# Kernel tuning notes

Measured on AMD Instinct MI355X. Metric: run time of the kernel, lower is better.

The kernel has to match this reference:

```python
import jax, jax.numpy as jnp
import numpy as np

B, N, C = 4, 49152, 256
E = 393216
CMID = C // 4
K = 3
EPS = 1e-5


def _cheb_prop(x, row, col, a_norm):
    # L_hat x with lambda_max=2, sym norm: L_hat = -D^{-1/2} A D^{-1/2} (zero diag)
    # x: [B, N, F]
    msg = a_norm[None, :, None] * x[:, col, :]           # [B, E, F]
    return -jnp.zeros_like(x).at[:, row, :].add(msg)


def _cheb_conv(x, row, col, a_norm, W, b):
    # W: [K, Fin, Fout], b: [Fout]
    out = jnp.einsum('bnf,fg->bng', x, W[0])
    Tx0, Tx1 = x, _cheb_prop(x, row, col, a_norm)
    out = out + jnp.einsum('bnf,fg->bng', Tx1, W[1])
    for k in range(2, W.shape[0]):
        Tx2 = 2.0 * _cheb_prop(Tx1, row, col, a_norm) - Tx0
        out = out + jnp.einsum('bnf,fg->bng', Tx2, W[k])
        Tx0, Tx1 = Tx1, Tx2
    return out + b


def _inst_norm(y):
    # InstanceNorm over the node axis (y viewed as [B, C, N]), affine=False
    mean = jnp.mean(y, axis=1, keepdims=True)
    var = jnp.var(y, axis=1, keepdims=True)
    return (y - mean) * jax.lax.rsqrt(var + EPS)


def setup_inputs() -> dict:
    key = jax.random.key(0)
    ks = jax.random.split(key, 8)
    x = jax.random.normal(ks[0], (B, N, C), dtype=jnp.float32)
    edge_index = jax.random.randint(ks[1], (2, E), 0, N, dtype=jnp.int32)
    edge_weight = jax.random.uniform(ks[2], (E,), dtype=jnp.float32)
    s1 = 1.0 / np.sqrt(C)
    s2 = 1.0 / np.sqrt(CMID)
    W1 = jax.random.normal(ks[3], (K, C, CMID), dtype=jnp.float32) * s1
    W2 = jax.random.normal(ks[4], (K, CMID, CMID), dtype=jnp.float32) * s2
    W3 = jax.random.normal(ks[5], (K, CMID, C), dtype=jnp.float32) * s2
    b1 = jnp.zeros((CMID,), dtype=jnp.float32)
    b2 = jnp.zeros((CMID,), dtype=jnp.float32)
    b3 = jnp.zeros((C,), dtype=jnp.float32)
    return {"x": x, "edge_index": edge_index, "edge_weight": edge_weight,
            "W1": W1, "b1": b1, "W2": W2, "b2": b2, "W3": W3, "b3": b3}


def reference(x, edge_index, edge_weight, W1, b1, W2, b2, W3, b3):
    row, col = edge_index[0], edge_index[1]
    deg = jnp.zeros((N,), dtype=x.dtype).at[row].add(edge_weight)
    dinv = jnp.where(deg > 0, jax.lax.rsqrt(jnp.maximum(deg, EPS)), 0.0)
    a_norm = edge_weight * dinv[row] * dinv[col]

    y = _cheb_conv(x, row, col, a_norm, W1, b1)
    y = jax.nn.relu(_inst_norm(y))
    y = _cheb_conv(y, row, col, a_norm, W2, b2)
    y = jax.nn.relu(_inst_norm(y))
    y = _cheb_conv(y, row, col, a_norm, W3, b3)
    y = jax.nn.relu(_inst_norm(y))
    return y + x
```

## Files before the change

### kernel.cpp

```cpp
#include <hip/hip_runtime.h>

#define NNODES 49152
#define NB 4
#define NE 393216
#define MTOT (NB*NNODES)
#define EPS 1e-5f

typedef __attribute__((ext_vector_type(8))) short s8v;
typedef __attribute__((ext_vector_type(4))) float f32x4;

__device__ inline float b2f(ushort u){ union{uint i; float f;} v; v.i = ((uint)u)<<16; return v.f; }
__device__ inline ushort f2b(float f){ union{float f; uint i;} v; v.f=f; uint r = v.i + 0x7fff + ((v.i>>16)&1); return (ushort)(r>>16); }

__global__ __launch_bounds__(256) void k_deg_cnt(const int* __restrict__ row,
    const float* __restrict__ w, float* __restrict__ deg, int* __restrict__ cnt)
{
    int e = blockIdx.x*256 + threadIdx.x;
    if (e >= NE) return;
    int r = row[e];
    atomicAdd(&deg[r], w[e]);
    atomicAdd(&cnt[r], 1);
}

__global__ __launch_bounds__(256) void k_dinv(const float* __restrict__ deg, float* __restrict__ dinv)
{
    int i = blockIdx.x*256 + threadIdx.x;
    if (i >= NNODES) return;
    float d = deg[i];
    dinv[i] = (d > 0.0f) ? rsqrtf(fmaxf(d, EPS)) : 0.0f;
}

__global__ __launch_bounds__(1024) void k_scan(const int* __restrict__ cnt, int* __restrict__ rowptr)
{
    __shared__ int ssum[1024];
    const int CH = NNODES/1024;
    int t = threadIdx.x;
    int base = t*CH;
    int loc[CH];
    int s = 0;
    #pragma unroll
    for (int i = 0; i < CH; ++i) { loc[i] = s; s += cnt[base+i]; }
    ssum[t] = s;
    __syncthreads();
    for (int off = 1; off < 1024; off <<= 1) {
        int v = ssum[t];
        int add = (t >= off) ? ssum[t-off] : 0;
        __syncthreads();
        ssum[t] = v + add;
        __syncthreads();
    }
    int prefix = (t == 0) ? 0 : ssum[t-1];
    #pragma unroll
    for (int i = 0; i < CH; ++i) rowptr[base+i] = prefix + loc[i];
    if (t == 0) rowptr[NNODES] = ssum[1023];
}

__global__ __launch_bounds__(256) void k_fill(const int* __restrict__ row, const int* __restrict__ col,
    const float* __restrict__ w, const float* __restrict__ dinv,
    const int* __restrict__ rowptr, int* __restrict__ fill,
    int* __restrict__ ecol, float* __restrict__ ea)
{
    int e = blockIdx.x*256 + threadIdx.x;
    if (e >= NE) return;
    int r = row[e], c = col[e];
    int pos = rowptr[r] + atomicAdd(&fill[r], 1);
    ecol[pos] = c;
    ea[pos] = w[e] * dinv[r] * dinv[c];
}

__global__ __launch_bounds__(256) void k_packB(const float* __restrict__ W, int Fin, int NF, int K,
    int mode, ushort* __restrict__ out)
{
    int t = blockIdx.x*256 + threadIdx.x;
    int lane = t & 63;
    int fid = t >> 6;
    if (fid >= (K/32)*NF) return;
    int kb = fid / NF, nb = fid % NF;
    int kbase = kb*32 + ((lane>>4)<<3);
    int n0 = nb*16 + (lane&15);
    #pragma unroll
    for (int j = 0; j < 8; ++j) {
        int kk = kbase + j;
        float v;
        if (mode == 0) {
            if (n0 < 64)       v = W[kk*64 + n0] - W[2*Fin*64 + kk*64 + n0];
            else if (n0 < 128) v = W[Fin*64 + kk*64 + (n0-64)];
            else               v = W[2*Fin*64 + kk*64 + (n0-128)];
        } else {
            v = W[(kk>>6)*64*256 + (kk&63)*256 + n0];
        }
        out[((long)fid*64 + lane)*8 + j] = f2b(v);
    }
}

__global__ __launch_bounds__(256) void k_gemm1(const float* __restrict__ A,
    const ushort* __restrict__ Bp, ushort* __restrict__ C0, ushort* __restrict__ C1, ushort* __restrict__ C2)
{
    int tid = threadIdx.x;
    int w = tid >> 6, l = tid & 63;
    int lr = l & 15, kg = l >> 4;
    int n0 = blockIdx.x * 32;
    f32x4 acc[2][12];
    #pragma unroll
    for (int rf = 0; rf < 2; ++rf)
        #pragma unroll
        for (int nb = 0; nb < 12; ++nb) acc[rf][nb] = (f32x4){0.f,0.f,0.f,0.f};

    for (int kt = 0; kt < 256; kt += 32) {
        s8v afr[2];
        #pragma unroll
        for (int rf = 0; rf < 2; ++rf) {
            long rowg = (long)w*NNODES + n0 + rf*16 + lr;
            const float* af = A + rowg*256 + kt + (kg<<3);
            float4 v0 = *(const float4*)af;
            float4 v1 = *(const float4*)(af + 4);
            s8v fr;
            fr[0]=(short)f2b(v0.x); fr[1]=(short)f2b(v0.y); fr[2]=(short)f2b(v0.z); fr[3]=(short)f2b(v0.w);
            fr[4]=(short)f2b(v1.x); fr[5]=(short)f2b(v1.y); fr[6]=(short)f2b(v1.z); fr[7]=(short)f2b(v1.w);
            afr[rf] = fr;
        }
        const ushort* bb = Bp + ((long)(kt>>5)*12)*512 + l*8;
        #pragma unroll
        for (int nb = 0; nb < 12; ++nb) {
            s8v bfr = *(const s8v*)(bb + nb*512);
            acc[0][nb] = __builtin_amdgcn_mfma_f32_16x16x32_bf16(afr[0], bfr, acc[0][nb], 0, 0, 0);
            acc[1][nb] = __builtin_amdgcn_mfma_f32_16x16x32_bf16(afr[1], bfr, acc[1][nb], 0, 0, 0);
        }
    }
    #pragma unroll
    for (int rf = 0; rf < 2; ++rf) {
        #pragma unroll
        for (int nb = 0; nb < 12; ++nb) {
            ushort* arr = (nb < 4) ? C0 : ((nb < 8) ? C1 : C2);
            #pragma unroll
            for (int i = 0; i < 4; ++i) {
                long crow = ((long)(n0 + rf*16 + kg*4 + i))*4 + w;
                arr[crow*64 + (nb&3)*16 + lr] = f2b(acc[rf][nb][i]);
            }
        }
    }
}

__global__ __launch_bounds__(256) void k_gemm2(const ushort* __restrict__ A,
    const ushort* __restrict__ Bp, ushort* __restrict__ C0, ushort* __restrict__ C1, ushort* __restrict__ C2)
{
    int tid = threadIdx.x;
    int w = tid >> 6, l = tid & 63;
    int lr = l & 15, kg = l >> 4;
    long rb = (long)blockIdx.x * 128;
    f32x4 acc[2][12];
    #pragma unroll
    for (int rf = 0; rf < 2; ++rf)
        #pragma unroll
        for (int nb = 0; nb < 12; ++nb) acc[rf][nb] = (f32x4){0.f,0.f,0.f,0.f};

    #pragma unroll
    for (int kt = 0; kt < 64; kt += 32) {
        s8v afr[2];
        #pragma unroll
        for (int rf = 0; rf < 2; ++rf) {
            long rg = rb + w*32 + rf*16 + lr;
            afr[rf] = *(const s8v*)(A + rg*64 + kt + (kg<<3));
        }
        const ushort* bb = Bp + ((long)(kt>>5)*12)*512 + l*8;
        #pragma unroll
        for (int nb = 0; nb < 12; ++nb) {
            s8v bfr = *(const s8v*)(bb + nb*512);
            acc[0][nb] = __builtin_amdgcn_mfma_f32_16x16x32_bf16(afr[0], bfr, acc[0][nb], 0, 0, 0);
            acc[1][nb] = __builtin_amdgcn_mfma_f32_16x16x32_bf16(afr[1], bfr, acc[1][nb], 0, 0, 0);
        }
    }
    #pragma unroll
    for (int rf = 0; rf < 2; ++rf) {
        #pragma unroll
        for (int nb = 0; nb < 12; ++nb) {
            ushort* arr = (nb < 4) ? C0 : ((nb < 8) ? C1 : C2);
            #pragma unroll
            for (int i = 0; i < 4; ++i) {
                long crow = rb + w*32 + rf*16 + kg*4 + i;
                arr[crow*64 + (nb&3)*16 + lr] = f2b(acc[rf][nb][i]);
            }
        }
    }
}

__global__ __launch_bounds__(256) void k_gemm3(const ushort* __restrict__ A0,
    const ushort* __restrict__ A1, const ushort* __restrict__ A2,
    const ushort* __restrict__ Bp, ushort* __restrict__ C, float* __restrict__ Pst)
{
    int tid = threadIdx.x;
    int w = tid >> 6, l = tid & 63;
    int lr = l & 15, kg = l >> 4;
    long rb = (long)blockIdx.x * 128;
    f32x4 acc[2][16];
    #pragma unroll
    for (int rf = 0; rf < 2; ++rf)
        #pragma unroll
        for (int nb = 0; nb < 16; ++nb) acc[rf][nb] = (f32x4){0.f,0.f,0.f,0.f};

    for (int kt = 0; kt < 192; kt += 32) {
        int part = kt >> 6, kc = kt & 63;
        const ushort* Ap = (part == 0) ? A0 : ((part == 1) ? A1 : A2);
        s8v afr[2];
        #pragma unroll
        for (int rf = 0; rf < 2; ++rf) {
            long rg = rb + w*32 + rf*16 + lr;
            afr[rf] = *(const s8v*)(Ap + rg*64 + kc + (kg<<3));
        }
        const ushort* bb = Bp + ((long)(kt>>5)*16)*512 + l*8;
        #pragma unroll
        for (int nb = 0; nb < 16; ++nb) {
            s8v bfr = *(const s8v*)(bb + nb*512);
            acc[0][nb] = __builtin_amdgcn_mfma_f32_16x16x32_bf16(afr[0], bfr, acc[0][nb], 0, 0, 0);
            acc[1][nb] = __builtin_amdgcn_mfma_f32_16x16x32_bf16(afr[1], bfr, acc[1][nb], 0, 0, 0);
        }
    }
    #pragma unroll
    for (int rf = 0; rf < 2; ++rf) {
        #pragma unroll
        for (int nb = 0; nb < 16; ++nb) {
            #pragma unroll
            for (int i = 0; i < 4; ++i) {
                long crow = rb + w*32 + rf*16 + kg*4 + i;
                C[crow*256 + nb*16 + lr] = f2b(acc[rf][nb][i]);
            }
        }
    }
    __shared__ float Ls[4][4][256];
    __shared__ float Lq[4][4][256];
    #pragma unroll
    for (int nb = 0; nb < 16; ++nb) {
        #pragma unroll
        for (int i = 0; i < 4; ++i) {
            float x0 = acc[0][nb][i], x1 = acc[1][nb][i];
            float s = x0 + x1;
            float q = x0*x0 + x1*x1;
            s += __shfl_xor(s, 16); s += __shfl_xor(s, 32);
            q += __shfl_xor(q, 16); q += __shfl_xor(q, 32);
            if (kg == 0) { Ls[w][i][nb*16 + lr] = s; Lq[w][i][nb*16 + lr] = q; }
        }
    }
    __syncthreads();
    int t = tid;
    #pragma unroll
    for (int b = 0; b < 4; ++b) {
        float S = Ls[0][b][t] + Ls[1][b][t] + Ls[2][b][t] + Ls[3][b][t];
        float Q = Lq[0][b][t] + Lq[1][b][t] + Lq[2][b][t] + Lq[3][b][t];
        Pst[(long)blockIdx.x*2048 + b*256 + t] = S;
        Pst[(long)blockIdx.x*2048 + 1024 + b*256 + t] = Q;
    }
}

__global__ __launch_bounds__(256) void k_prop(
    const int* __restrict__ rowptr, const int* __restrict__ ecol, const float* __restrict__ ea,
    const ushort* __restrict__ src, const ushort* __restrict__ basep, float beta,
    ushort* __restrict__ dst, float alpha, float* __restrict__ Pst)
{
    int g = blockIdx.x*8 + (threadIdx.x >> 5);
    int sub = threadIdx.x & 31;
    int e0 = rowptr[g], e1 = rowptr[g+1];
    float acc[8];
    #pragma unroll
    for (int j = 0; j < 8; ++j) acc[j] = 0.f;
    int e = e0;
    for (; e + 4 <= e1; e += 4) {
        int c0 = ecol[e], c1 = ecol[e+1], c2 = ecol[e+2], c3 = ecol[e+3];
        float a0 = ea[e], a1 = ea[e+1], a2 = ea[e+2], a3 = ea[e+3];
        s8v v0 = *(const s8v*)(src + (long)c0*256 + sub*8);
        s8v v1 = *(const s8v*)(src + (long)c1*256 + sub*8);
        s8v v2 = *(const s8v*)(src + (long)c2*256 + sub*8);
        s8v v3 = *(const s8v*)(src + (long)c3*256 + sub*8);
        #pragma unroll
        for (int j = 0; j < 8; ++j)
            acc[j] += a0*b2f((ushort)v0[j]) + a1*b2f((ushort)v1[j])
                    + a2*b2f((ushort)v2[j]) + a3*b2f((ushort)v3[j]);
    }
    for (; e < e1; ++e) {
        int c = ecol[e]; float a = ea[e];
        s8v v = *(const s8v*)(src + (long)c*256 + sub*8);
        #pragma unroll
        for (int j = 0; j < 8; ++j) acc[j] += a*b2f((ushort)v[j]);
    }
    float o[8];
    if (basep) {
        s8v bv = *(const s8v*)(basep + (long)g*256 + sub*8);
        #pragma unroll
        for (int j = 0; j < 8; ++j) o[j] = alpha*acc[j] + beta*b2f((ushort)bv[j]);
    } else {
        #pragma unroll
        for (int j = 0; j < 8; ++j) o[j] = alpha*acc[j];
    }
    s8v ov;
    #pragma unroll
    for (int j = 0; j < 8; ++j) ov[j] = (short)f2b(o[j]);
    *(s8v*)(dst + (long)g*256 + sub*8) = ov;

    if (Pst) {
        __shared__ float Ls[8][256];
        __shared__ float Lq[8][256];
        int grp = threadIdx.x >> 5;
        #pragma unroll
        for (int j = 0; j < 8; ++j) {
            Ls[grp][sub*8 + j] = o[j];
            Lq[grp][sub*8 + j] = o[j]*o[j];
        }
        __syncthreads();
        int t = threadIdx.x;
        float s = 0.f, q = 0.f;
        #pragma unroll
        for (int k = 0; k < 8; ++k) { s += Ls[k][t]; q += Lq[k][t]; }
        Pst[(long)blockIdx.x*512 + t] = s;
        Pst[(long)blockIdx.x*512 + 256 + t] = q;
    }
}

__global__ __launch_bounds__(256) void k_redgen(const float* __restrict__ in, float* __restrict__ out,
    int S, int nin)
{
    int j = blockIdx.x*256 + threadIdx.x;
    int o = blockIdx.y;
    long base = (long)o*nin*S + j;
    float s = 0.f;
    for (int k = 0; k < nin; ++k) s += in[base + (long)k*S];
    out[(long)o*S + j] = s;
}

__global__ __launch_bounds__(256) void k_redfin(const float* __restrict__ in, int S, int nin, int Cw,
    float* __restrict__ mean, float* __restrict__ rs)
{
    int half = S >> 1;
    int j = blockIdx.x*256 + threadIdx.x;
    if (j >= half) return;
    float s = 0.f, q = 0.f;
    for (int k = 0; k < nin; ++k) {
        s += in[(long)k*S + j];
        q += in[(long)k*S + half + j];
    }
    float m = s / (float)NNODES;
    float v = q / (float)NNODES - m*m;
    int b = j / Cw, c = j - b*Cw;
    mean[b*256 + c] = m;
    rs[b*256 + c] = rsqrtf(v + EPS);
}

__global__ __launch_bounds__(256) void k_normrelu(const ushort* __restrict__ y,
    const float* __restrict__ mean, const float* __restrict__ rs, ushort* __restrict__ X)
{
    int t = threadIdx.x;
    long e = (long)blockIdx.x*2048 + t*8;
    int b = (t>>3)&3, c0 = (t&7)*8;
    s8v v = *(const s8v*)(y + e);
    float4 m0 = *(const float4*)(mean + b*256 + c0);
    float4 m1 = *(const float4*)(mean + b*256 + c0 + 4);
    float4 r0 = *(const float4*)(rs + b*256 + c0);
    float4 r1 = *(const float4*)(rs + b*256 + c0 + 4);
    float mm[8] = {m0.x,m0.y,m0.z,m0.w,m1.x,m1.y,m1.z,m1.w};
    float rr[8] = {r0.x,r0.y,r0.z,r0.w,r1.x,r1.y,r1.z,r1.w};
    s8v o;
    #pragma unroll
    for (int j = 0; j < 8; ++j) o[j] = (short)f2b(fmaxf((b2f((ushort)v[j]) - mm[j])*rr[j], 0.f));
    *(s8v*)(X + e) = o;
}

__global__ __launch_bounds__(256) void k_final(const ushort* __restrict__ Ybf,
    const float* __restrict__ x, const float* __restrict__ mean, const float* __restrict__ rs,
    float* __restrict__ out)
{
    int t = threadIdx.x;
    long orow = (long)blockIdx.x*8 + (t>>5);
    int c0 = (t&31)*8;
    int b = (int)(orow / NNODES);
    int n = (int)(orow - (long)b*NNODES);
    s8v v = *(const s8v*)(Ybf + ((long)n*4 + b)*256 + c0);
    float4 m0 = *(const float4*)(mean + b*256 + c0);
    float4 m1 = *(const float4*)(mean + b*256 + c0 + 4);
    float4 r0 = *(const float4*)(rs + b*256 + c0);
    float4 r1 = *(const float4*)(rs + b*256 + c0 + 4);
    float mm[8] = {m0.x,m0.y,m0.z,m0.w,m1.x,m1.y,m1.z,m1.w};
    float rr[8] = {r0.x,r0.y,r0.z,r0.w,r1.x,r1.y,r1.z,r1.w};
    const float* xp = x + orow*256 + c0;
    float* op = out + orow*256 + c0;
    #pragma unroll
    for (int j = 0; j < 8; ++j)
        op[j] = fmaxf((b2f((ushort)v[j]) - mm[j])*rr[j], 0.f) + xp[j];
}

extern "C" void kernel_launch(void* const* d_in, const int* in_sizes, int n_in,
                              void* d_out, int out_size, void* d_ws, size_t ws_size,
                              hipStream_t stream)
{
    const float* x  = (const float*)d_in[0];
    const int*   ei = (const int*)d_in[1];
    const float* ew = (const float*)d_in[2];
    const float* W1 = (const float*)d_in[3];
    const float* W2 = (const float*)d_in[5];
    const float* W3 = (const float*)d_in[7];
    const int* row = ei;
    const int* col = ei + NE;

    char* p = (char*)d_ws;
    size_t used = 0;
    auto alloc = [&](size_t bytes) -> void* {
        void* r = p + used;
        used += (bytes + 1023) & ~(size_t)1023;
        return r;
    };
    float* deg   = (float*)alloc((size_t)3*NNODES*4);
    int*   cnt   = (int*)(deg + NNODES);
    int*   fillc = (int*)(deg + 2*NNODES);
    float* dinv  = (float*)alloc((size_t)NNODES*4);
    int*   rowptr= (int*)alloc((size_t)(NNODES+1)*4);
    int*   ecol  = (int*)alloc((size_t)NE*4);
    float* ea    = (float*)alloc((size_t)NE*4);
    float* mrs   = (float*)alloc((size_t)3*2*1024*4);
    ushort* Bp1  = (ushort*)alloc((size_t)256*192*2);
    ushort* Bp2  = (ushort*)alloc((size_t)64*192*2);
    ushort* Bp3  = (ushort*)alloc((size_t)192*256*2);
    ushort* Za   = (ushort*)alloc((size_t)MTOT*64*2);
    ushort* Zb   = (ushort*)alloc((size_t)MTOT*64*2);
    ushort* Zc   = (ushort*)alloc((size_t)MTOT*64*2);
    ushort* Zd   = (ushort*)alloc((size_t)MTOT*64*2);
    float* Pbig  = (float*)alloc((size_t)6144*512*4);
    float* PPa   = (float*)alloc((size_t)256*2048*4);
    float* PPb   = (float*)alloc((size_t)16*2048*4);
    ushort* Ybf  = (ushort*)alloc((size_t)MTOT*256*2);
    if (ws_size < used) return;

    float* mean1 = mrs;          float* rs1 = mrs + 1024;
    float* mean2 = mrs + 2048;   float* rs2 = mrs + 3072;
    float* mean3 = mrs + 4096;   float* rs3 = mrs + 5120;

    hipMemsetAsync(deg, 0, (size_t)3*NNODES*4, stream);
    k_deg_cnt<<<NE/256, 256, 0, stream>>>(row, ew, deg, cnt);
    k_dinv<<<NNODES/256, 256, 0, stream>>>(deg, dinv);
    k_scan<<<1, 1024, 0, stream>>>(cnt, rowptr);
    k_fill<<<NE/256, 256, 0, stream>>>(row, col, ew, dinv, rowptr, fillc, ecol, ea);
    k_packB<<<24, 256, 0, stream>>>(W1, 256, 12, 256, 0, Bp1);
    k_packB<<<6, 256, 0, stream>>>(W2, 64, 12, 64, 0, Bp2);
    k_packB<<<24, 256, 0, stream>>>(W3, 64, 16, 192, 1, Bp3);

    k_gemm1<<<NNODES/32, 256, 0, stream>>>(x, Bp1, Za, Zb, Zc);
    k_prop<<<NNODES/8, 256, 0, stream>>>(rowptr, ecol, ea, Zc, Zb, 1.f, Zb, -2.f, nullptr);
    k_prop<<<NNODES/8, 256, 0, stream>>>(rowptr, ecol, ea, Zb, Za, 1.f, Za, -1.f, Pbig);
    k_redgen<<<dim3(2,512), 256, 0, stream>>>(Pbig, PPa, 512, 12);
    k_redgen<<<dim3(2,32), 256, 0, stream>>>(PPa, PPb, 512, 16);
    k_redfin<<<1, 256, 0, stream>>>(PPb, 512, 32, 64, mean1, rs1);
    k_normrelu<<<MTOT*64/2048, 256, 0, stream>>>(Za, mean1, rs1, Zc);

    k_gemm2<<<MTOT/128, 256, 0, stream>>>(Zc, Bp2, Za, Zb, Zd);
    k_prop<<<NNODES/8, 256, 0, stream>>>(rowptr, ecol, ea, Zd, Zb, 1.f, Zb, -2.f, nullptr);
    k_prop<<<NNODES/8, 256, 0, stream>>>(rowptr, ecol, ea, Zb, Za, 1.f, Za, -1.f, Pbig);
    k_redgen<<<dim3(2,512), 256, 0, stream>>>(Pbig, PPa, 512, 12);
    k_redgen<<<dim3(2,32), 256, 0, stream>>>(PPa, PPb, 512, 16);
    k_redfin<<<1, 256, 0, stream>>>(PPb, 512, 32, 64, mean2, rs2);
    k_normrelu<<<MTOT*64/2048, 256, 0, stream>>>(Za, mean2, rs2, Zc);

    k_prop<<<NNODES/8, 256, 0, stream>>>(rowptr, ecol, ea, Zc, (const ushort*)nullptr, 0.f, Za, -1.f, nullptr);
    k_prop<<<NNODES/8, 256, 0, stream>>>(rowptr, ecol, ea, Za, Zc, -1.f, Zb, -2.f, nullptr);
    k_gemm3<<<MTOT/128, 256, 0, stream>>>(Zc, Za, Zb, Bp3, Ybf, Pbig);
    k_redgen<<<dim3(8,256), 256, 0, stream>>>(Pbig, PPa, 2048, 6);
    k_redgen<<<dim3(8,16), 256, 0, stream>>>(PPa, PPb, 2048, 16);
    k_redfin<<<4, 256, 0, stream>>>(PPb, 2048, 16, 256, mean3, rs3);
    k_final<<<MTOT/8, 256, 0, stream>>>(Ybf, x, mean3, rs3, (float*)d_out);
}
```

Before: 717.0 us.

## Stage GEMM weights in double-buffered LDS and halve per-block row tiles

All three GEMM kernels now stage the packed weight matrix in shared memory, double-buffered with register prefetch for gemm1 and gemm3, instead of each wave reading B fragments from global memory. Each block now covers half as many rows (one 16-row fragment per wave), and launch bounds request three blocks per SM. This lowers register pressure, raises occupancy and cuts redundant global B traffic, at the cost of more blocks and more syncs. The gemm3 partial-stat buffer moves into the output buffer, which doubles the partial count fed to the reduction.

```diff
diff --git a/kernel.cpp b/kernel.cpp
--- a/kernel.cpp
+++ b/kernel.cpp
@@ -93,161 +93,185 @@
     }
 }
 
-__global__ __launch_bounds__(256) void k_gemm1(const float* __restrict__ A,
+__global__ __launch_bounds__(256,3) void k_gemm1(const float* __restrict__ A,
     const ushort* __restrict__ Bp, ushort* __restrict__ C0, ushort* __restrict__ C1, ushort* __restrict__ C2)
 {
+    __shared__ ushort Bs[2][6144];
     int tid = threadIdx.x;
     int w = tid >> 6, l = tid & 63;
     int lr = l & 15, kg = l >> 4;
-    int n0 = blockIdx.x * 32;
-    f32x4 acc[2][12];
-    #pragma unroll
-    for (int rf = 0; rf < 2; ++rf)
-        #pragma unroll
-        for (int nb = 0; nb < 12; ++nb) acc[rf][nb] = (f32x4){0.f,0.f,0.f,0.f};
-
-    for (int kt = 0; kt < 256; kt += 32) {
-        s8v afr[2];
-        #pragma unroll
-        for (int rf = 0; rf < 2; ++rf) {
-            long rowg = (long)w*NNODES + n0 + rf*16 + lr;
-            const float* af = A + rowg*256 + kt + (kg<<3);
-            float4 v0 = *(const float4*)af;
-            float4 v1 = *(const float4*)(af + 4);
-            s8v fr;
-            fr[0]=(short)f2b(v0.x); fr[1]=(short)f2b(v0.y); fr[2]=(short)f2b(v0.z); fr[3]=(short)f2b(v0.w);
-            fr[4]=(short)f2b(v1.x); fr[5]=(short)f2b(v1.y); fr[6]=(short)f2b(v1.z); fr[7]=(short)f2b(v1.w);
-            afr[rf] = fr;
-        }
-        const ushort* bb = Bp + ((long)(kt>>5)*12)*512 + l*8;
+    int n0 = blockIdx.x * 16;
+
+    const float* ap = A + ((long)w*NNODES + n0 + lr)*256 + (kg<<3);
+    s8v af[8];
+    #pragma unroll
+    for (int t = 0; t < 8; ++t) {
+        float4 v0 = *(const float4*)(ap + t*32);
+        float4 v1 = *(const float4*)(ap + t*32 + 4);
+        s8v fr;
+        fr[0]=(short)f2b(v0.x); fr[1]=(short)f2b(v0.y); fr[2]=(short)f2b(v0.z); fr[3]=(short)f2b(v0.w);
+        fr[4]=(short)f2b(v1.x); fr[5]=(short)f2b(v1.y); fr[6]=(short)f2b(v1.z); fr[7]=(short)f2b(v1.w);
+        af[t] = fr;
+    }
+    f32x4 acc[12];
+    #pragma unroll
+    for (int nb = 0; nb < 12; ++nb) acc[nb] = (f32x4){0.f,0.f,0.f,0.f};
+
+    #pragma unroll
+    for (int ps = 0; ps < 3; ++ps) {
+        int off = ps*2048 + tid*8;
+        *(s8v*)(&Bs[0][off]) = *(const s8v*)(Bp + off);
+    }
+    #pragma unroll
+    for (int t = 0; t < 8; ++t) {
+        __syncthreads();
+        s8v stg[3];
+        if (t < 7) {
+            #pragma unroll
+            for (int ps = 0; ps < 3; ++ps)
+                stg[ps] = *(const s8v*)(Bp + (long)(t+1)*6144 + ps*2048 + tid*8);
+        }
+        const ushort* bb = &Bs[t&1][l*8];
         #pragma unroll
         for (int nb = 0; nb < 12; ++nb) {
             s8v bfr = *(const s8v*)(bb + nb*512);
-            acc[0][nb] = __builtin_amdgcn_mfma_f32_16x16x32_bf16(afr[0], bfr, acc[0][nb], 0, 0, 0);
-            acc[1][nb] = __builtin_amdgcn_mfma_f32_16x16x32_bf16(afr[1], bfr, acc[1][nb], 0, 0, 0);
-        }
-    }
-    #pragma unroll
-    for (int rf = 0; rf < 2; ++rf) {
-        #pragma unroll
-        for (int nb = 0; nb < 12; ++nb) {
-            ushort* arr = (nb < 4) ? C0 : ((nb < 8) ? C1 : C2);
+            acc[nb] = __builtin_amdgcn_mfma_f32_16x16x32_bf16(af[t], bfr, acc[nb], 0, 0, 0);
+        }
+        if (t < 7) {
             #pragma unroll
-            for (int i = 0; i < 4; ++i) {
-                long crow = ((long)(n0 + rf*16 + kg*4 + i))*4 + w;
-                arr[crow*64 + (nb&3)*16 + lr] = f2b(acc[rf][nb][i]);
-            }
-        }
-    }
-}
-
-__global__ __launch_bounds__(256) void k_gemm2(const ushort* __restrict__ A,
+            for (int ps = 0; ps < 3; ++ps)
+                *(s8v*)(&Bs[(t+1)&1][ps*2048 + tid*8]) = stg[ps];
+        }
+    }
+    #pragma unroll
+    for (int nb = 0; nb < 12; ++nb) {
+        ushort* arr = (nb < 4) ? C0 : ((nb < 8) ? C1 : C2);
+        int cc = (nb&3)*16 + lr;
+        #pragma unroll
+        for (int i = 0; i < 4; ++i) {
+            long crow = (long)(n0 + kg*4 + i)*4 + w;
+            arr[crow*64 + cc] = f2b(acc[nb][i]);
+        }
+    }
+}
+
+__global__ __launch_bounds__(256,3) void k_gemm2(const ushort* __restrict__ A,
     const ushort* __restrict__ Bp, ushort* __restrict__ C0, ushort* __restrict__ C1, ushort* __restrict__ C2)
 {
+    __shared__ ushort Bs[12288];
     int tid = threadIdx.x;
     int w = tid >> 6, l = tid & 63;
     int lr = l & 15, kg = l >> 4;
-    long rb = (long)blockIdx.x * 128;
-    f32x4 acc[2][12];
-    #pragma unroll
-    for (int rf = 0; rf < 2; ++rf)
-        #pragma unroll
-        for (int nb = 0; nb < 12; ++nb) acc[rf][nb] = (f32x4){0.f,0.f,0.f,0.f};
-
-    #pragma unroll
-    for (int kt = 0; kt < 64; kt += 32) {
-        s8v afr[2];
-        #pragma unroll
-        for (int rf = 0; rf < 2; ++rf) {
-            long rg = rb + w*32 + rf*16 + lr;
-            afr[rf] = *(const s8v*)(A + rg*64 + kt + (kg<<3));
-        }
-        const ushort* bb = Bp + ((long)(kt>>5)*12)*512 + l*8;
+    long rb = (long)blockIdx.x * 64;
+
+    long arow = (rb + w*16 + lr)*64 + (kg<<3);
+    s8v af0 = *(const s8v*)(A + arow);
+    s8v af1 = *(const s8v*)(A + arow + 32);
+    #pragma unroll
+    for (int ps = 0; ps < 6; ++ps) {
+        int off = ps*2048 + tid*8;
+        *(s8v*)(&Bs[off]) = *(const s8v*)(Bp + off);
+    }
+    f32x4 acc[12];
+    #pragma unroll
+    for (int nb = 0; nb < 12; ++nb) acc[nb] = (f32x4){0.f,0.f,0.f,0.f};
+    __syncthreads();
+    #pragma unroll
+    for (int t = 0; t < 2; ++t) {
+        const ushort* bb = &Bs[t*6144 + l*8];
+        s8v afr = t ? af1 : af0;
         #pragma unroll
         for (int nb = 0; nb < 12; ++nb) {
             s8v bfr = *(const s8v*)(bb + nb*512);
-            acc[0][nb] = __builtin_amdgcn_mfma_f32_16x16x32_bf16(afr[0], bfr, acc[0][nb], 0, 0, 0);
-            acc[1][nb] = __builtin_amdgcn_mfma_f32_16x16x32_bf16(afr[1], bfr, acc[1][nb], 0, 0, 0);
-        }
-    }
-    #pragma unroll
-    for (int rf = 0; rf < 2; ++rf) {
-        #pragma unroll
-        for (int nb = 0; nb < 12; ++nb) {
-            ushort* arr = (nb < 4) ? C0 : ((nb < 8) ? C1 : C2);
-            #pragma unroll
-            for (int i = 0; i < 4; ++i) {
-                long crow = rb + w*32 + rf*16 + kg*4 + i;
-                arr[crow*64 + (nb&3)*16 + lr] = f2b(acc[rf][nb][i]);
-            }
-        }
-    }
-}
-
-__global__ __launch_bounds__(256) void k_gemm3(const ushort* __restrict__ A0,
+            acc[nb] = __builtin_amdgcn_mfma_f32_16x16x32_bf16(afr, bfr, acc[nb], 0, 0, 0);
+        }
+    }
+    #pragma unroll
+    for (int nb = 0; nb < 12; ++nb) {
+        ushort* arr = (nb < 4) ? C0 : ((nb < 8) ? C1 : C2);
+        int cc = (nb&3)*16 + lr;
+        #pragma unroll
+        for (int i = 0; i < 4; ++i) {
+            long crow = rb + w*16 + kg*4 + i;
+            arr[crow*64 + cc] = f2b(acc[nb][i]);
+        }
+    }
+}
+
+__global__ __launch_bounds__(256,3) void k_gemm3(const ushort* __restrict__ A0,
     const ushort* __restrict__ A1, const ushort* __restrict__ A2,
     const ushort* __restrict__ Bp, ushort* __restrict__ C, float* __restrict__ Pst)
 {
+    __shared__ ushort Bs[2][8192];
     int tid = threadIdx.x;
     int w = tid >> 6, l = tid & 63;
     int lr = l & 15, kg = l >> 4;
-    long rb = (long)blockIdx.x * 128;
-    f32x4 acc[2][16];
-    #pragma unroll
-    for (int rf = 0; rf < 2; ++rf)
-        #pragma unroll
-        for (int nb = 0; nb < 16; ++nb) acc[rf][nb] = (f32x4){0.f,0.f,0.f,0.f};
-
-    for (int kt = 0; kt < 192; kt += 32) {
-        int part = kt >> 6, kc = kt & 63;
-        const ushort* Ap = (part == 0) ? A0 : ((part == 1) ? A1 : A2);
-        s8v afr[2];
-        #pragma unroll
-        for (int rf = 0; rf < 2; ++rf) {
-            long rg = rb + w*32 + rf*16 + lr;
-            afr[rf] = *(const s8v*)(Ap + rg*64 + kc + (kg<<3));
-        }
-        const ushort* bb = Bp + ((long)(kt>>5)*16)*512 + l*8;
+    long rb = (long)blockIdx.x * 64;
+
+    long arow = (rb + w*16 + lr)*64 + (kg<<3);
+    s8v ap[6];
+    ap[0] = *(const s8v*)(A0 + arow); ap[1] = *(const s8v*)(A0 + arow + 32);
+    ap[2] = *(const s8v*)(A1 + arow); ap[3] = *(const s8v*)(A1 + arow + 32);
+    ap[4] = *(const s8v*)(A2 + arow); ap[5] = *(const s8v*)(A2 + arow + 32);
+    f32x4 acc[16];
+    #pragma unroll
+    for (int nb = 0; nb < 16; ++nb) acc[nb] = (f32x4){0.f,0.f,0.f,0.f};
+
+    #pragma unroll
+    for (int ps = 0; ps < 4; ++ps) {
+        int off = ps*2048 + tid*8;
+        *(s8v*)(&Bs[0][off]) = *(const s8v*)(Bp + off);
+    }
+    #pragma unroll
+    for (int t = 0; t < 6; ++t) {
+        __syncthreads();
+        s8v stg[4];
+        if (t < 5) {
+            #pragma unroll
+            for (int ps = 0; ps < 4; ++ps)
+                stg[ps] = *(const s8v*)(Bp + (long)(t+1)*8192 + ps*2048 + tid*8);
+        }
+        const ushort* bb = &Bs[t&1][l*8];
         #pragma unroll
         for (int nb = 0; nb < 16; ++nb) {
             s8v bfr = *(const s8v*)(bb + nb*512);
-            acc[0][nb] = __builtin_amdgcn_mfma_f32_16x16x32_bf16(afr[0], bfr, acc[0][nb], 0, 0, 0);
-            acc[1][nb] = __builtin_amdgcn_mfma_f32_16x16x32_bf16(afr[1], bfr, acc[1][nb], 0, 0, 0);
-        }
-    }
-    #pragma unroll
-    for (int rf = 0; rf < 2; ++rf) {
-        #pragma unroll
-        for (int nb = 0; nb < 16; ++nb) {
+            acc[nb] = __builtin_amdgcn_mfma_f32_16x16x32_bf16(ap[t], bfr, acc[nb], 0, 0, 0);
+        }
+        if (t < 5) {
             #pragma unroll
-            for (int i = 0; i < 4; ++i) {
-                long crow = rb + w*32 + rf*16 + kg*4 + i;
-                C[crow*256 + nb*16 + lr] = f2b(acc[rf][nb][i]);
-            }
-        }
-    }
-    __shared__ float Ls[4][4][256];
-    __shared__ float Lq[4][4][256];
+            for (int ps = 0; ps < 4; ++ps)
+                *(s8v*)(&Bs[(t+1)&1][ps*2048 + tid*8]) = stg[ps];
+        }
+    }
     #pragma unroll
     for (int nb = 0; nb < 16; ++nb) {
         #pragma unroll
         for (int i = 0; i < 4; ++i) {
-            float x0 = acc[0][nb][i], x1 = acc[1][nb][i];
-            float s = x0 + x1;
-            float q = x0*x0 + x1*x1;
+            long crow = rb + w*16 + kg*4 + i;
+            C[crow*256 + nb*16 + lr] = f2b(acc[nb][i]);
+        }
+    }
+    __syncthreads();
+    float* Ls = (float*)Bs;
+    float* Lq = Ls + 4096;
+    #pragma unroll
+    for (int nb = 0; nb < 16; ++nb) {
+        #pragma unroll
+        for (int i = 0; i < 4; ++i) {
+            float s = acc[nb][i];
+            float q = s*s;
             s += __shfl_xor(s, 16); s += __shfl_xor(s, 32);
             q += __shfl_xor(q, 16); q += __shfl_xor(q, 32);
-            if (kg == 0) { Ls[w][i][nb*16 + lr] = s; Lq[w][i][nb*16 + lr] = q; }
+            if (kg == 0) { Ls[(w*4 + i)*256 + nb*16 + lr] = s; Lq[(w*4 + i)*256 + nb*16 + lr] = q; }
         }
     }
     __syncthreads();
-    int t = tid;
     #pragma unroll
     for (int b = 0; b < 4; ++b) {
-        float S = Ls[0][b][t] + Ls[1][b][t] + Ls[2][b][t] + Ls[3][b][t];
-        float Q = Lq[0][b][t] + Lq[1][b][t] + Lq[2][b][t] + Lq[3][b][t];
-        Pst[(long)blockIdx.x*2048 + b*256 + t] = S;
-        Pst[(long)blockIdx.x*2048 + 1024 + b*256 + t] = Q;
+        float S = Ls[b*256 + tid] + Ls[(4+b)*256 + tid] + Ls[(8+b)*256 + tid] + Ls[(12+b)*256 + tid];
+        float Q = Lq[b*256 + tid] + Lq[(4+b)*256 + tid] + Lq[(8+b)*256 + tid] + Lq[(12+b)*256 + tid];
+        Pst[(long)blockIdx.x*2048 + b*256 + tid] = S;
+        Pst[(long)blockIdx.x*2048 + 1024 + b*256 + tid] = Q;
     }
 }
 
@@ -429,6 +453,7 @@
     float* mean1 = mrs;          float* rs1 = mrs + 1024;
     float* mean2 = mrs + 2048;   float* rs2 = mrs + 3072;
     float* mean3 = mrs + 4096;   float* rs3 = mrs + 5120;
+    float* Pst3  = (float*)d_out;
 
     hipMemsetAsync(deg, 0, (size_t)3*NNODES*4, stream);
     k_deg_cnt<<<NE/256, 256, 0, stream>>>(row, ew, deg, cnt);
@@ -439,7 +464,7 @@
     k_packB<<<6, 256, 0, stream>>>(W2, 64, 12, 64, 0, Bp2);
     k_packB<<<24, 256, 0, stream>>>(W3, 64, 16, 192, 1, Bp3);
 
-    k_gemm1<<<NNODES/32, 256, 0, stream>>>(x, Bp1, Za, Zb, Zc);
+    k_gemm1<<<NNODES/16, 256, 0, stream>>>(x, Bp1, Za, Zb, Zc);
     k_prop<<<NNODES/8, 256, 0, stream>>>(rowptr, ecol, ea, Zc, Zb, 1.f, Zb, -2.f, nullptr);
     k_prop<<<NNODES/8, 256, 0, stream>>>(rowptr, ecol, ea, Zb, Za, 1.f, Za, -1.f, Pbig);
     k_redgen<<<dim3(2,512), 256, 0, stream>>>(Pbig, PPa, 512, 12);
@@ -447,7 +472,7 @@
     k_redfin<<<1, 256, 0, stream>>>(PPb, 512, 32, 64, mean1, rs1);
     k_normrelu<<<MTOT*64/2048, 256, 0, stream>>>(Za, mean1, rs1, Zc);
 
-    k_gemm2<<<MTOT/128, 256, 0, stream>>>(Zc, Bp2, Za, Zb, Zd);
+    k_gemm2<<<MTOT/64, 256, 0, stream>>>(Zc, Bp2, Za, Zb, Zd);
     k_prop<<<NNODES/8, 256, 0, stream>>>(rowptr, ecol, ea, Zd, Zb, 1.f, Zb, -2.f, nullptr);
     k_prop<<<NNODES/8, 256, 0, stream>>>(rowptr, ecol, ea, Zb, Za, 1.f, Za, -1.f, Pbig);
     k_redgen<<<dim3(2,512), 256, 0, stream>>>(Pbig, PPa, 512, 12);
@@ -457,8 +482,8 @@
 
     k_prop<<<NNODES/8, 256, 0, stream>>>(rowptr, ecol, ea, Zc, (const ushort*)nullptr, 0.f, Za, -1.f, nullptr);
     k_prop<<<NNODES/8, 256, 0, stream>>>(rowptr, ecol, ea, Za, Zc, -1.f, Zb, -2.f, nullptr);
-    k_gemm3<<<MTOT/128, 256, 0, stream>>>(Zc, Za, Zb, Bp3, Ybf, Pbig);
-    k_redgen<<<dim3(8,256), 256, 0, stream>>>(Pbig, PPa, 2048, 6);
+    k_gemm3<<<MTOT/64, 256, 0, stream>>>(Zc, Za, Zb, Bp3, Ybf, Pst3);
+    k_redgen<<<dim3(8,256), 256, 0, stream>>>(Pst3, PPa, 2048, 12);
     k_redgen<<<dim3(8,16), 256, 0, stream>>>(PPa, PPb, 2048, 16);
     k_redfin<<<4, 256, 0, stream>>>(PPb, 2048, 16, 256, mean3, rs3);
     k_final<<<MTOT/8, 256, 0, stream>>>(Ybf, x, mean3, rs3, (float*)d_out);
```

Result: faster. 618.9 us (-13.7%).
